# Optimization experiments

Hardware: AMD Instinct MI355X
Metric: run time of the kernel (lower is better)

## Reference

```python
import jax, jax.numpy as jnp
import numpy as np

NUM_HEADS = 10
LN_EPS = 1e-5

def setup_inputs() -> dict:
    key = jax.random.key(0)
    ks = jax.random.split(key, 8)
    B, H, N, D, Dt = 256, 200, 64, 640, 256
    s = 0.02
    return {
        'clicked_news': jax.random.normal(ks[0], (B, H, D), jnp.float32),
        'clicked_topics': jax.random.normal(ks[1], (B, H, Dt), jnp.float32),
        'cand_topics': jax.random.normal(ks[2], (B, N, Dt), jnp.float32),
        'Wq': jax.random.normal(ks[3], (D, Dt), jnp.float32) * s,
        'bq': jnp.zeros((D,), jnp.float32),
        'Wk': jax.random.normal(ks[4], (D, Dt), jnp.float32) * s,
        'bk': jnp.zeros((D,), jnp.float32),
        'Wv': jax.random.normal(ks[5], (D, D), jnp.float32) * s,
        'bv': jnp.zeros((D,), jnp.float32),
        'Wg': jax.random.normal(ks[6], (D, D), jnp.float32) * s,
        'bg': jnp.zeros((D,), jnp.float32),
        'ln_gamma': jnp.ones((D,), jnp.float32),
        'ln_beta': jnp.zeros((D,), jnp.float32),
    }

def reference(clicked_news, clicked_topics, cand_topics, Wq, bq, Wk, bk, Wv, bv, Wg, bg, ln_gamma, ln_beta):
    B, H, D = clicked_news.shape
    N = cand_topics.shape[1]
    nh = NUM_HEADS
    hd = D // nh
    scale = jnp.sqrt(jnp.asarray(D, clicked_news.dtype))

    Qf = cand_topics @ Wq.T + bq            # [B, N, D]
    Kf = clicked_topics @ Wk.T + bk         # [B, H, D]
    # V projection feeds `weighted`, which is dead code w.r.t. outputs; omitted.

    Q = Qf.reshape(B, N, nh, hd)
    K = Kf.reshape(B, H, nh, hd)
    scores = jnp.einsum('bnhd,bmhd->bhnm', Q, K) / scale   # [B, nh, N, H]
    attn = jax.nn.softmax(scores, axis=-1)                 # dropout is identity in eval

    # query weighting: softmax over candidates of ||Q||
    query_weights = jax.nn.softmax(jnp.linalg.norm(Qf, axis=-1), axis=1)   # [B, N]
    agg = (attn.sum(axis=1) * query_weights[:, :, None]).sum(axis=1)       # [B, H]
    attn_weights_agg = jax.nn.softmax(agg, axis=-1)                        # [B, H]

    weighted_clicked = attn_weights_agg[:, :, None] * clicked_news         # [B, H, D]
    gate = jax.nn.sigmoid(weighted_clicked @ Wg.T + bg)
    out = gate * weighted_clicked + (1.0 - gate) * clicked_news

    mu = out.mean(axis=-1, keepdims=True)
    var = out.var(axis=-1, keepdims=True)
    out = (out - mu) / jnp.sqrt(var + LN_EPS) * ln_gamma + ln_beta
    return out, attn_weights_agg
```

## Files before the change

### kernel.cpp

```cpp
#include <hip/hip_runtime.h>
#include <math.h>

#define B_  256
#define H_  200
#define N_  64
#define D_  640
#define DT_ 256
#define NH_ 10
#define HD_ 64
#define MT_ 13

typedef __attribute__((ext_vector_type(8))) short bf16x8;
typedef __attribute__((ext_vector_type(4))) float f32x4;

__device__ __forceinline__ float wave_reduce_sum(float v) {
    #pragma unroll
    for (int m = 32; m > 0; m >>= 1) v += __shfl_xor(v, m);
    return v;
}
__device__ __forceinline__ float wave_reduce_max(float v) {
    #pragma unroll
    for (int m = 32; m > 0; m >>= 1) v = fmaxf(v, __shfl_xor(v, m));
    return v;
}
__device__ __forceinline__ float red16_sum(float v) {
    #pragma unroll
    for (int m = 1; m < 16; m <<= 1) v += __shfl_xor(v, m);
    return v;
}
__device__ __forceinline__ float red16_max(float v) {
    #pragma unroll
    for (int m = 1; m < 16; m <<= 1) v = fmaxf(v, __shfl_xor(v, m));
    return v;
}
__device__ __forceinline__ short f2bf(float x) {
    unsigned u = __float_as_uint(x);
    unsigned r = (u + 0x7fffu + ((u >> 16) & 1u)) >> 16;
    return (short)r;
}
__device__ __forceinline__ float bf2f(short s) {
    return __uint_as_float(((unsigned)(unsigned short)s) << 16);
}
#define SWZ(row, byte) ((byte) ^ (((row) & 7) << 4))
#define WSWZ_S(col, sidx) ((sidx) ^ ((((col) >> 1) & 3) << 3))

__device__ __forceinline__ void gload_lds16(const void* g, void* lds) {
    __builtin_amdgcn_global_load_lds(
        (const __attribute__((address_space(1))) void*)g,
        (__attribute__((address_space(3))) void*)lds, 16, 0, 0);
}

__global__ __launch_bounds__(256) void convert_w(
    const float* __restrict__ src, short* __restrict__ dst, int n)
{
    for (int i = blockIdx.x * 256 + threadIdx.x; i < n; i += gridDim.x * 256)
        dst[i] = f2bf(src[i]);
}

__global__ __launch_bounds__(256) void convert_wg(
    const float* __restrict__ src, short* __restrict__ dst)
{
    for (int i = blockIdx.x * 256 + threadIdx.x; i < D_ * D_; i += gridDim.x * 256) {
        const int col = i / D_, k = i % D_;
        const int kc = k >> 5, kk = k & 31;
        dst[kc * (D_ * 32) + WSWZ_S(col, col * 32 + kk)] = f2bf(src[i]);
    }
}

__global__ __launch_bounds__(512, 2) void proj_mfma(
    const float* __restrict__ X, const short* __restrict__ Wb,
    const float* __restrict__ bias, short* __restrict__ Y)
{
    __shared__ short A_lds[64 * DT_];
    const int t = threadIdx.x;
    const int lane = t & 63, w = t >> 6;
    const int r16 = lane & 15, g = lane >> 4;
    const long row0 = (long)blockIdx.x * 64;

    {
        const int srow = t >> 3, sc = t & 7;
        const float4* src = (const float4*)(X + (row0 + srow) * DT_) + sc;
        float4 sv[8];
        #pragma unroll
        for (int j = 0; j < 8; ++j) sv[j] = src[8 * j];
        #pragma unroll
        for (int j = 0; j < 8; ++j) {
            short4 s;
            s.x = f2bf(sv[j].x); s.y = f2bf(sv[j].y);
            s.z = f2bf(sv[j].z); s.w = f2bf(sv[j].w);
            *(short4*)((char*)A_lds + SWZ(srow, srow * (DT_ * 2) + (sc + 8 * j) * 8)) = s;
        }
    }
    __syncthreads();

    f32x4 acc[5][4];
    #pragma unroll
    for (int ct = 0; ct < 5; ++ct)
        #pragma unroll
        for (int rt = 0; rt < 4; ++rt) acc[ct][rt] = (f32x4){0.f,0.f,0.f,0.f};

    const short* Wbase = Wb + (long)(w * 80 + r16) * DT_ + g * 8;

    bf16x8 aA[4], bA[5], aB[4], bB[5];
    #pragma unroll
    for (int rt = 0; rt < 4; ++rt) {
        const int row = rt * 16 + r16;
        aA[rt] = *(const bf16x8*)((const char*)A_lds + SWZ(row, row * (DT_ * 2) + g * 16));
    }
    #pragma unroll
    for (int ct = 0; ct < 5; ++ct) bA[ct] = *(const bf16x8*)(Wbase + ct * 16 * DT_);

    #pragma unroll
    for (int kc = 0; kc < 8; kc += 2) {
        {
            const int kn = kc + 1;
            #pragma unroll
            for (int rt = 0; rt < 4; ++rt) {
                const int row = rt * 16 + r16;
                aB[rt] = *(const bf16x8*)((const char*)A_lds +
                          SWZ(row, row * (DT_ * 2) + kn * 64 + g * 16));
            }
            #pragma unroll
            for (int ct = 0; ct < 5; ++ct)
                bB[ct] = *(const bf16x8*)(Wbase + ct * 16 * DT_ + kn * 32);
        }
        #pragma unroll
        for (int ct = 0; ct < 5; ++ct)
            #pragma unroll
            for (int rt = 0; rt < 4; ++rt)
                acc[ct][rt] = __builtin_amdgcn_mfma_f32_16x16x32_bf16(
                                  aA[rt], bA[ct], acc[ct][rt], 0, 0, 0);
        {
            const int kn = (kc + 2 < 8) ? kc + 2 : 0;
            #pragma unroll
            for (int rt = 0; rt < 4; ++rt) {
                const int row = rt * 16 + r16;
                aA[rt] = *(const bf16x8*)((const char*)A_lds +
                          SWZ(row, row * (DT_ * 2) + kn * 64 + g * 16));
            }
            #pragma unroll
            for (int ct = 0; ct < 5; ++ct)
                bA[ct] = *(const bf16x8*)(Wbase + ct * 16 * DT_ + kn * 32);
        }
        #pragma unroll
        for (int ct = 0; ct < 5; ++ct)
            #pragma unroll
            for (int rt = 0; rt < 4; ++rt)
                acc[ct][rt] = __builtin_amdgcn_mfma_f32_16x16x32_bf16(
                                  aB[rt], bB[ct], acc[ct][rt], 0, 0, 0);
    }

    #pragma unroll
    for (int ct = 0; ct < 5; ++ct) {
        const int col = w * 80 + ct * 16 + r16;
        const float bv = bias[col];
        #pragma unroll
        for (int rt = 0; rt < 4; ++rt)
            #pragma unroll
            for (int i = 0; i < 4; ++i)
                Y[(row0 + rt * 16 + g * 4 + i) * (long)D_ + col] =
                    f2bf(acc[ct][rt][i] + bv);
    }
}

__global__ __launch_bounds__(512, 2) void attn2(
    const short* __restrict__ Qb, const short* __restrict__ Kb,
    float* __restrict__ aw, float* __restrict__ out_tail)
{
    __shared__ float qn_l[N_];
    __shared__ float qw_l[N_];
    __shared__ float aggp[8][MT_ * 16];
    __shared__ float red2[2];
    const int t = threadIdx.x;
    const int lane = t & 63, w = t >> 6;
    const int wm = w & 3, hh = w >> 2;
    const int r16 = lane & 15, g = lane >> 4;
    const int b = blockIdx.x;

    if (hh == 0) {
        const short* qrow = Qb + ((long)(b * N_ + wm * 16 + r16)) * D_ + g * 160;
        float ss = 0.f;
        #pragma unroll
        for (int j = 0; j < 20; ++j) {
            bf16x8 v = *(const bf16x8*)(qrow + j * 8);
            #pragma unroll
            for (int e = 0; e < 8; ++e) { float f = bf2f(v[e]); ss += f * f; }
        }
        ss += __shfl_xor(ss, 16);
        ss += __shfl_xor(ss, 32);
        if (g == 0) qn_l[wm * 16 + r16] = ss;
    }
    __syncthreads();
    if (w == 0) {
        float v = sqrtf(qn_l[lane]);
        float mx = wave_reduce_max(v);
        float e = __expf(v - mx);
        float s = wave_reduce_sum(e);
        qw_l[lane] = e / s;
    }
    __syncthreads();

    float qwr[4];
    #pragma unroll
    for (int i = 0; i < 4; ++i) qwr[i] = qw_l[wm * 16 + g * 4 + i];

    const float inv_scale = 0.0395284707521047f;
    float aggl[MT_];
    #pragma unroll
    for (int mt = 0; mt < MT_; ++mt) aggl[mt] = 0.f;

    for (int hi = 0; hi < 5; ++hi) {
        const int h = hh * 5 + hi;
        const short* qbase = Qb + ((long)(b * N_ + wm * 16 + r16)) * D_ + h * HD_ + g * 8;
        bf16x8 a0 = *(const bf16x8*)(qbase);
        bf16x8 a1 = *(const bf16x8*)(qbase + 32);
        bf16x8 kb0[MT_], kb1[MT_];
        #pragma unroll
        for (int mt = 0; mt < MT_; ++mt) {
            const short* kbase = Kb + ((long)(b * H_ + mt * 16 + r16)) * D_ + h * HD_ + g * 8;
            kb0[mt] = *(const bf16x8*)(kbase);
            kb1[mt] = *(const bf16x8*)(kbase + 32);
        }
        f32x4 acc[MT_];
        #pragma unroll
        for (int mt = 0; mt < MT_; ++mt) {
            f32x4 z = {0.f,0.f,0.f,0.f};
            z = __builtin_amdgcn_mfma_f32_16x16x32_bf16(a0, kb0[mt], z, 0, 0, 0);
            z = __builtin_amdgcn_mfma_f32_16x16x32_bf16(a1, kb1[mt], z, 0, 0, 0);
            acc[mt] = z;
        }
        const bool tailok = (r16 < 8);
        float mx[4] = {-INFINITY, -INFINITY, -INFINITY, -INFINITY};
        #pragma unroll
        for (int mt = 0; mt < MT_; ++mt) {
            const bool valid = (mt < 12) || tailok;
            #pragma unroll
            for (int i = 0; i < 4; ++i)
                if (valid) mx[i] = fmaxf(mx[i], acc[mt][i]);
        }
        #pragma unroll
        for (int i = 0; i < 4; ++i) mx[i] = red16_max(mx[i]);
        float sum[4] = {0.f, 0.f, 0.f, 0.f};
        #pragma unroll
        for (int mt = 0; mt < MT_; ++mt) {
            const bool valid = (mt < 12) || tailok;
            #pragma unroll
            for (int i = 0; i < 4; ++i) {
                float e = valid ? __expf((acc[mt][i] - mx[i]) * inv_scale) : 0.f;
                acc[mt][i] = e;
                sum[i] += e;
            }
        }
        float fct[4];
        #pragma unroll
        for (int i = 0; i < 4; ++i) fct[i] = qwr[i] / red16_sum(sum[i]);
        #pragma unroll
        for (int mt = 0; mt < MT_; ++mt)
            aggl[mt] += acc[mt][0] * fct[0] + acc[mt][1] * fct[1]
                      + acc[mt][2] * fct[2] + acc[mt][3] * fct[3];
    }
    #pragma unroll
    for (int mt = 0; mt < MT_; ++mt) {
        aggl[mt] += __shfl_xor(aggl[mt], 16);
        aggl[mt] += __shfl_xor(aggl[mt], 32);
    }
    if (g == 0) {
        #pragma unroll
        for (int mt = 0; mt < MT_; ++mt) aggp[w][mt * 16 + r16] = aggl[mt];
    }
    __syncthreads();
    if (t < MT_ * 16) {
        float v = 0.f;
        #pragma unroll
        for (int j = 0; j < 8; ++j) v += aggp[j][t];
        aggp[0][t] = v;
    }
    __syncthreads();
    if (w == 0) {
        float v0 = aggp[0][lane], v1 = aggp[0][lane + 64], v2 = aggp[0][lane + 128];
        const bool has3 = lane < (H_ - 192);
        float v3 = has3 ? aggp[0][lane + 192] : -INFINITY;
        float mx = wave_reduce_max(fmaxf(fmaxf(v0, v1), fmaxf(v2, v3)));
        float s = __expf(v0 - mx) + __expf(v1 - mx) + __expf(v2 - mx)
                + (has3 ? __expf(v3 - mx) : 0.f);
        s = wave_reduce_sum(s);
        if (lane == 0) { red2[0] = mx; red2[1] = s; }
    }
    __syncthreads();
    if (t < H_) {
        float v = __expf(aggp[0][t] - red2[0]) / red2[1];
        aw[b * H_ + t] = v;
        out_tail[b * H_ + t] = v;
    }
}

__global__ __launch_bounds__(512, 2) void out_mfma(
    const float* __restrict__ clicked, const float* __restrict__ aw,
    const short* __restrict__ Wgb, const float* __restrict__ bg,
    const float* __restrict__ gamma, const float* __restrict__ beta,
    float* __restrict__ out, float* __restrict__ part_g)
{
    __shared__ short A_lds[64 * D_];
    __shared__ short W_lds[2][D_ * 32];
    const int t = threadIdx.x;
    const int lane = t & 63, w = t >> 6;
    const int r16 = lane & 15, g = lane >> 4;
    const int bid = blockIdx.x;
    const long row0 = (long)bid * 64;

    float bgr[5], gmr[5], btr[5];
    #pragma unroll
    for (int ct = 0; ct < 5; ++ct) {
        const int col = w * 80 + ct * 16 + r16;
        bgr[ct] = bg[col]; gmr[ct] = gamma[col]; btr[ct] = beta[col];
    }

    const int arow = t >> 3, aseg = t & 7;
    const float* Asrc = clicked + (row0 + arow) * D_ + aseg * 4;

    f32x4 acc[5][4];
    #pragma unroll
    for (int ct = 0; ct < 5; ++ct)
        #pragma unroll
        for (int rt = 0; rt < 4; ++rt) acc[ct][rt] = (f32x4){0.f,0.f,0.f,0.f};

    float4 av = *(const float4*)(Asrc);
    {
        const short* wsrc = Wgb;
        #pragma unroll
        for (int j = 0; j < 5; ++j) {
            const int u = t + j * 512;
            gload_lds16(wsrc + u * 8, (char*)W_lds[0] + u * 16);
        }
    }
    {
        short4 s;
        s.x = f2bf(av.x); s.y = f2bf(av.y); s.z = f2bf(av.z); s.w = f2bf(av.w);
        *(short4*)((char*)A_lds + SWZ(arow, arow * (D_ * 2) + 0 * 64 + aseg * 8)) = s;
    }
    av = *(const float4*)(Asrc + 32);
    __syncthreads();

    int cur = 0;
    for (int k = 0; k < 20; ++k) {
        const int nxt = cur ^ 1;
        if (k + 1 < 20) {
            const short* wsrc = Wgb + (long)(k + 1) * (D_ * 32);
            #pragma unroll
            for (int j = 0; j < 5; ++j) {
                const int u = t + j * 512;
                gload_lds16(wsrc + u * 8, (char*)W_lds[nxt] + u * 16);
            }
            short4 s;
            s.x = f2bf(av.x); s.y = f2bf(av.y); s.z = f2bf(av.z); s.w = f2bf(av.w);
            *(short4*)((char*)A_lds +
                SWZ(arow, arow * (D_ * 2) + (k + 1) * 64 + aseg * 8)) = s;
        }
        if (k + 2 < 20) av = *(const float4*)(Asrc + (k + 2) * 32);

        bf16x8 a[4];
        #pragma unroll
        for (int rt = 0; rt < 4; ++rt) {
            const int row = rt * 16 + r16;
            a[rt] = *(const bf16x8*)((const char*)A_lds +
                     SWZ(row, row * (D_ * 2) + k * 64 + g * 16));
        }
        bf16x8 bb[5];
        #pragma unroll
        for (int ct = 0; ct < 5; ++ct) {
            const int c3 = w * 80 + ct * 16 + r16;
            bb[ct] = *(const bf16x8*)((const short*)W_lds[cur] +
                      WSWZ_S(c3, c3 * 32 + g * 8));
        }
        #pragma unroll
        for (int ct = 0; ct < 5; ++ct)
            #pragma unroll
            for (int rt = 0; rt < 4; ++rt)
                acc[ct][rt] = __builtin_amdgcn_mfma_f32_16x16x32_bf16(
                                  a[rt], bb[ct], acc[ct][rt], 0, 0, 0);
        __syncthreads();
        cur = nxt;
    }

    float awv[4][4];
    #pragma unroll
    for (int rt = 0; rt < 4; ++rt)
        #pragma unroll
        for (int i = 0; i < 4; ++i)
            awv[rt][i] = aw[row0 + rt * 16 + g * 4 + i];

    float ps[4][4], pq[4][4];
    #pragma unroll
    for (int rt = 0; rt < 4; ++rt)
        #pragma unroll
        for (int i = 0; i < 4; ++i) { ps[rt][i] = 0.f; pq[rt][i] = 0.f; }

    #pragma unroll
    for (int ct = 0; ct < 5; ++ct) {
        const int col = w * 80 + ct * 16 + r16;
        #pragma unroll
        for (int rt = 0; rt < 4; ++rt)
            #pragma unroll
            for (int i = 0; i < 4; ++i) {
                const int row = rt * 16 + g * 4 + i;
                const float awr = awv[rt][i];
                const float cl = bf2f(*(const short*)((const char*)A_lds +
                                   SWZ(row, row * (D_ * 2) + col * 2)));
                const float z  = awr * acc[ct][rt][i] + bgr[ct];
                const float gt = 1.f / (1.f + __expf(-z));
                const float o  = cl * (1.f + gt * (awr - 1.f));
                acc[ct][rt][i] = o;
                ps[rt][i] += o; pq[rt][i] += o * o;
            }
    }
    float* pg = part_g + (long)bid * 1280;
    #pragma unroll
    for (int rt = 0; rt < 4; ++rt)
        #pragma unroll
        for (int i = 0; i < 4; ++i) {
            const float s  = red16_sum(ps[rt][i]);
            const float sq = red16_sum(pq[rt][i]);
            if (r16 == 0) {
                const int row = rt * 16 + g * 4 + i;
                pg[(w * 64 + row) * 2 + 0] = s;
                pg[(w * 64 + row) * 2 + 1] = sq;
            }
        }
    __syncthreads();
    if (t < 64) {
        float s = 0.f, q = 0.f;
        #pragma unroll
        for (int j = 0; j < 8; ++j) {
            s += pg[(j * 64 + t) * 2 + 0];
            q += pg[(j * 64 + t) * 2 + 1];
        }
        const float m = s * (1.f / D_);
        const float v = q * (1.f / D_) - m * m;
        pg[1024 + t * 2 + 0] = m;
        pg[1024 + t * 2 + 1] = 1.0f / sqrtf(v + 1e-5f);
    }
    __syncthreads();

    #pragma unroll
    for (int rt = 0; rt < 4; ++rt)
        #pragma unroll
        for (int i = 0; i < 4; ++i) {
            const int row = rt * 16 + g * 4 + i;
            const float mu = pg[1024 + row * 2 + 0];
            const float ri = pg[1024 + row * 2 + 1];
            #pragma unroll
            for (int ct = 0; ct < 5; ++ct) {
                const int col = w * 80 + ct * 16 + r16;
                out[(row0 + row) * (long)D_ + col] =
                    (acc[ct][rt][i] - mu) * ri * gmr[ct] + btr[ct];
            }
        }
}

extern "C" void kernel_launch(void* const* d_in, const int* in_sizes, int n_in,
                              void* d_out, int out_size, void* d_ws, size_t ws_size,
                              hipStream_t stream) {
    const float* clicked_news   = (const float*)d_in[0];
    const float* clicked_topics = (const float*)d_in[1];
    const float* cand_topics    = (const float*)d_in[2];
    const float* Wq = (const float*)d_in[3];
    const float* bq = (const float*)d_in[4];
    const float* Wk = (const float*)d_in[5];
    const float* bk = (const float*)d_in[6];
    const float* Wg = (const float*)d_in[9];
    const float* bg = (const float*)d_in[10];
    const float* ln_gamma = (const float*)d_in[11];
    const float* ln_beta  = (const float*)d_in[12];

    float* out = (float*)d_out;
    float* ws  = (float*)d_ws;

    float* aw     = ws;
    float* part_g = aw + (long)B_ * H_;
    short* sbase  = (short*)(part_g + (long)800 * 1280);
    short* Qb   = sbase;
    short* Wq_b = Qb + (long)B_ * N_ * D_;
    short* Wg_b = Wq_b + (long)D_ * DT_;
    short* Wk_b = Wg_b + (long)D_ * D_;
    short* Kb = (short*)d_out;
    float* out_tail = out + (long)B_ * H_ * D_;

    convert_w<<<128, 256, 0, stream>>>(Wq, Wq_b, D_ * DT_);
    convert_w<<<128, 256, 0, stream>>>(Wk, Wk_b, D_ * DT_);
    convert_wg<<<256, 256, 0, stream>>>(Wg, Wg_b);

    proj_mfma<<<(B_ * N_) / 64, 512, 0, stream>>>(cand_topics, Wq_b, bq, Qb);
    proj_mfma<<<(B_ * H_) / 64, 512, 0, stream>>>(clicked_topics, Wk_b, bk, Kb);
    attn2<<<B_, 512, 0, stream>>>(Qb, Kb, aw, out_tail);
    out_mfma<<<(B_ * H_) / 64, 512, 0, stream>>>(clicked_news, aw, Wg_b, bg,
                                                 ln_gamma, ln_beta, out, part_g);
}
```

Baseline: 299.3 us.

## Shrink out_mfma tiles to 32 rows, stage fp32 A via async LDS loads

The gated-output GEMM kernel now processes 32 rows per block instead of 64. It keeps a single W buffer plus a small double-buffered fp32 A tile loaded with direct global-to-LDS copies and converted to bf16 at fragment-load time. LDS use drops sharply and launch bounds rise to allow 4 blocks per CU, aiming for higher occupancy and more blocks (1600). In exchange, every block re-streams the full Wg, the W loads are no longer overlapped across iterations, and the epilogue re-reads clicked_news from global memory instead of LDS.

New measurement: 295.8 us. About the same (-1.2%).

```diff
diff --git a/kernel.cpp b/kernel.cpp
--- a/kernel.cpp
+++ b/kernel.cpp
@@ -294,165 +294,139 @@
     }
 }
 
-__global__ __launch_bounds__(512, 2) void out_mfma(
+__global__ __launch_bounds__(512, 4) void out_mfma(
     const float* __restrict__ clicked, const float* __restrict__ aw,
     const short* __restrict__ Wgb, const float* __restrict__ bg,
     const float* __restrict__ gamma, const float* __restrict__ beta,
     float* __restrict__ out, float* __restrict__ part_g)
 {
-    __shared__ short A_lds[64 * D_];
-    __shared__ short W_lds[2][D_ * 32];
+    __shared__ short W_lds[D_ * 32];
+    __shared__ float Afp[2][32 * 32];
     const int t = threadIdx.x;
     const int lane = t & 63, w = t >> 6;
     const int r16 = lane & 15, g = lane >> 4;
     const int bid = blockIdx.x;
-    const long row0 = (long)bid * 64;
-
-    float bgr[5], gmr[5], btr[5];
+    const long row0 = (long)bid * 32;
+
+    f32x4 acc[5][2];
+    #pragma unroll
+    for (int ct = 0; ct < 5; ++ct) {
+        acc[ct][0] = (f32x4){0.f,0.f,0.f,0.f};
+        acc[ct][1] = (f32x4){0.f,0.f,0.f,0.f};
+    }
+
+    const int au_row = t >> 3, au_j = t & 7;
+    const float* Ag = clicked + (row0 + au_row) * (long)D_ + ((au_j ^ (au_row & 7)) * 4);
+
+    if (t < 256) gload_lds16(Ag + 0 * 32, (char*)Afp[0] + t * 16);
+
+    for (int k = 0; k < 20; ++k) {
+        {
+            const short* wsrc = Wgb + (long)k * (D_ * 32);
+            #pragma unroll
+            for (int j = 0; j < 5; ++j) {
+                const int u = t + j * 512;
+                gload_lds16(wsrc + u * 8, (char*)W_lds + u * 16);
+            }
+        }
+        if (k + 1 < 20 && t < 256)
+            gload_lds16(Ag + (k + 1) * 32, (char*)Afp[(k + 1) & 1] + t * 16);
+        __syncthreads();
+
+        const char* ab = (const char*)Afp[k & 1];
+        bf16x8 a[2];
+        #pragma unroll
+        for (int rt = 0; rt < 2; ++rt) {
+            const int row = rt * 16 + r16;
+            float4 f0 = *(const float4*)(ab + row * 128 + (((g * 2 + 0) ^ (row & 7)) * 16));
+            float4 f1 = *(const float4*)(ab + row * 128 + (((g * 2 + 1) ^ (row & 7)) * 16));
+            bf16x8 av;
+            av[0] = f2bf(f0.x); av[1] = f2bf(f0.y); av[2] = f2bf(f0.z); av[3] = f2bf(f0.w);
+            av[4] = f2bf(f1.x); av[5] = f2bf(f1.y); av[6] = f2bf(f1.z); av[7] = f2bf(f1.w);
+            a[rt] = av;
+        }
+        #pragma unroll
+        for (int ct = 0; ct < 5; ++ct) {
+            const int c3 = w * 80 + ct * 16 + r16;
+            bf16x8 bb = *(const bf16x8*)((const short*)W_lds +
+                         WSWZ_S(c3, c3 * 32 + g * 8));
+            acc[ct][0] = __builtin_amdgcn_mfma_f32_16x16x32_bf16(a[0], bb, acc[ct][0], 0, 0, 0);
+            acc[ct][1] = __builtin_amdgcn_mfma_f32_16x16x32_bf16(a[1], bb, acc[ct][1], 0, 0, 0);
+        }
+        __syncthreads();
+    }
+
+    float awv[2][4];
+    #pragma unroll
+    for (int rt = 0; rt < 2; ++rt)
+        #pragma unroll
+        for (int i = 0; i < 4; ++i)
+            awv[rt][i] = aw[row0 + rt * 16 + g * 4 + i];
+
+    float ps[2][4], pq[2][4];
+    #pragma unroll
+    for (int rt = 0; rt < 2; ++rt)
+        #pragma unroll
+        for (int i = 0; i < 4; ++i) { ps[rt][i] = 0.f; pq[rt][i] = 0.f; }
+
     #pragma unroll
     for (int ct = 0; ct < 5; ++ct) {
         const int col = w * 80 + ct * 16 + r16;
-        bgr[ct] = bg[col]; gmr[ct] = gamma[col]; btr[ct] = beta[col];
-    }
-
-    const int arow = t >> 3, aseg = t & 7;
-    const float* Asrc = clicked + (row0 + arow) * D_ + aseg * 4;
-
-    f32x4 acc[5][4];
-    #pragma unroll
-    for (int ct = 0; ct < 5; ++ct)
-        #pragma unroll
-        for (int rt = 0; rt < 4; ++rt) acc[ct][rt] = (f32x4){0.f,0.f,0.f,0.f};
-
-    float4 av = *(const float4*)(Asrc);
-    {
-        const short* wsrc = Wgb;
-        #pragma unroll
-        for (int j = 0; j < 5; ++j) {
-            const int u = t + j * 512;
-            gload_lds16(wsrc + u * 8, (char*)W_lds[0] + u * 16);
-        }
-    }
-    {
-        short4 s;
-        s.x = f2bf(av.x); s.y = f2bf(av.y); s.z = f2bf(av.z); s.w = f2bf(av.w);
-        *(short4*)((char*)A_lds + SWZ(arow, arow * (D_ * 2) + 0 * 64 + aseg * 8)) = s;
-    }
-    av = *(const float4*)(Asrc + 32);
-    __syncthreads();
-
-    int cur = 0;
-    for (int k = 0; k < 20; ++k) {
-        const int nxt = cur ^ 1;
-        if (k + 1 < 20) {
-            const short* wsrc = Wgb + (long)(k + 1) * (D_ * 32);
-            #pragma unroll
-            for (int j = 0; j < 5; ++j) {
-                const int u = t + j * 512;
-                gload_lds16(wsrc + u * 8, (char*)W_lds[nxt] + u * 16);
-            }
-            short4 s;
-            s.x = f2bf(av.x); s.y = f2bf(av.y); s.z = f2bf(av.z); s.w = f2bf(av.w);
-            *(short4*)((char*)A_lds +
-                SWZ(arow, arow * (D_ * 2) + (k + 1) * 64 + aseg * 8)) = s;
-        }
-        if (k + 2 < 20) av = *(const float4*)(Asrc + (k + 2) * 32);
-
-        bf16x8 a[4];
-        #pragma unroll
-        for (int rt = 0; rt < 4; ++rt) {
-            const int row = rt * 16 + r16;
-            a[rt] = *(const bf16x8*)((const char*)A_lds +
-                     SWZ(row, row * (D_ * 2) + k * 64 + g * 16));
-        }
-        bf16x8 bb[5];
-        #pragma unroll
-        for (int ct = 0; ct < 5; ++ct) {
-            const int c3 = w * 80 + ct * 16 + r16;
-            bb[ct] = *(const bf16x8*)((const short*)W_lds[cur] +
-                      WSWZ_S(c3, c3 * 32 + g * 8));
-        }
-        #pragma unroll
-        for (int ct = 0; ct < 5; ++ct)
-            #pragma unroll
-            for (int rt = 0; rt < 4; ++rt)
-                acc[ct][rt] = __builtin_amdgcn_mfma_f32_16x16x32_bf16(
-                                  a[rt], bb[ct], acc[ct][rt], 0, 0, 0);
-        __syncthreads();
-        cur = nxt;
-    }
-
-    float awv[4][4];
-    #pragma unroll
-    for (int rt = 0; rt < 4; ++rt)
-        #pragma unroll
-        for (int i = 0; i < 4; ++i)
-            awv[rt][i] = aw[row0 + rt * 16 + g * 4 + i];
-
-    float ps[4][4], pq[4][4];
-    #pragma unroll
-    for (int rt = 0; rt < 4; ++rt)
-        #pragma unroll
-        for (int i = 0; i < 4; ++i) { ps[rt][i] = 0.f; pq[rt][i] = 0.f; }
-
-    #pragma unroll
-    for (int ct = 0; ct < 5; ++ct) {
-        const int col = w * 80 + ct * 16 + r16;
-        #pragma unroll
-        for (int rt = 0; rt < 4; ++rt)
+        const float bgv = bg[col];
+        #pragma unroll
+        for (int rt = 0; rt < 2; ++rt)
             #pragma unroll
             for (int i = 0; i < 4; ++i) {
                 const int row = rt * 16 + g * 4 + i;
                 const float awr = awv[rt][i];
-                const float cl = bf2f(*(const short*)((const char*)A_lds +
-                                   SWZ(row, row * (D_ * 2) + col * 2)));
-                const float z  = awr * acc[ct][rt][i] + bgr[ct];
+                const float cl = clicked[(row0 + row) * (long)D_ + col];
+                const float z  = awr * acc[ct][rt][i] + bgv;
                 const float gt = 1.f / (1.f + __expf(-z));
                 const float o  = cl * (1.f + gt * (awr - 1.f));
                 acc[ct][rt][i] = o;
                 ps[rt][i] += o; pq[rt][i] += o * o;
             }
     }
-    float* pg = part_g + (long)bid * 1280;
-    #pragma unroll
-    for (int rt = 0; rt < 4; ++rt)
+    float* pg = part_g + (long)bid * 640;
+    #pragma unroll
+    for (int rt = 0; rt < 2; ++rt)
         #pragma unroll
         for (int i = 0; i < 4; ++i) {
             const float s  = red16_sum(ps[rt][i]);
             const float sq = red16_sum(pq[rt][i]);
             if (r16 == 0) {
                 const int row = rt * 16 + g * 4 + i;
-                pg[(w * 64 + row) * 2 + 0] = s;
-                pg[(w * 64 + row) * 2 + 1] = sq;
-            }
-        }
-    __syncthreads();
-    if (t < 64) {
+                pg[(w * 32 + row) * 2 + 0] = s;
+                pg[(w * 32 + row) * 2 + 1] = sq;
+            }
+        }
+    __syncthreads();
+    if (t < 32) {
         float s = 0.f, q = 0.f;
         #pragma unroll
         for (int j = 0; j < 8; ++j) {
-            s += pg[(j * 64 + t) * 2 + 0];
-            q += pg[(j * 64 + t) * 2 + 1];
+            s += pg[(j * 32 + t) * 2 + 0];
+            q += pg[(j * 32 + t) * 2 + 1];
         }
         const float m = s * (1.f / D_);
         const float v = q * (1.f / D_) - m * m;
-        pg[1024 + t * 2 + 0] = m;
-        pg[1024 + t * 2 + 1] = 1.0f / sqrtf(v + 1e-5f);
-    }
-    __syncthreads();
-
-    #pragma unroll
-    for (int rt = 0; rt < 4; ++rt)
+        pg[512 + t * 2 + 0] = m;
+        pg[512 + t * 2 + 1] = 1.0f / sqrtf(v + 1e-5f);
+    }
+    __syncthreads();
+
+    #pragma unroll
+    for (int rt = 0; rt < 2; ++rt)
         #pragma unroll
         for (int i = 0; i < 4; ++i) {
             const int row = rt * 16 + g * 4 + i;
-            const float mu = pg[1024 + row * 2 + 0];
-            const float ri = pg[1024 + row * 2 + 1];
+            const float mu = pg[512 + row * 2 + 0];
+            const float ri = pg[512 + row * 2 + 1];
             #pragma unroll
             for (int ct = 0; ct < 5; ++ct) {
                 const int col = w * 80 + ct * 16 + r16;
                 out[(row0 + row) * (long)D_ + col] =
-                    (acc[ct][rt][i] - mu) * ri * gmr[ct] + btr[ct];
+                    (acc[ct][rt][i] - mu) * ri * gamma[col] + beta[col];
             }
         }
 }
@@ -477,7 +451,7 @@
 
     float* aw     = ws;
     float* part_g = aw + (long)B_ * H_;
-    short* sbase  = (short*)(part_g + (long)800 * 1280);
+    short* sbase  = (short*)(part_g + (long)1600 * 640);
     short* Qb   = sbase;
     short* Wq_b = Qb + (long)B_ * N_ * D_;
     short* Wg_b = Wq_b + (long)D_ * DT_;
@@ -492,6 +466,6 @@
     proj_mfma<<<(B_ * N_) / 64, 512, 0, stream>>>(cand_topics, Wq_b, bq, Qb);
     proj_mfma<<<(B_ * H_) / 64, 512, 0, stream>>>(clicked_topics, Wk_b, bk, Kb);
     attn2<<<B_, 512, 0, stream>>>(Qb, Kb, aw, out_tail);
-    out_mfma<<<(B_ * H_) / 64, 512, 0, stream>>>(clicked_news, aw, Wg_b, bg,
+    out_mfma<<<(B_ * H_) / 32, 512, 0, stream>>>(clicked_news, aw, Wg_b, bg,
                                                  ln_gamma, ln_beta, out, part_g);
 }
```
